# Kernel tuning notes

Hardware: AMD Instinct MI355X
Metric: run time of the kernel (lower is better)

## Reference

```python
import jax, jax.numpy as jnp
import numpy as np

B = 64
H = 768  # hidden_dim; x is [B, H, H], split along dim 1 into Q, D of [B, H//2, H]


def setup_inputs() -> dict:
    key = jax.random.key(0)
    kx, kw, kb = jax.random.split(key, 3)
    x = jax.random.normal(kx, (B, H, H), dtype=jnp.float32)
    # nn.Linear(H, H): weight [out, in], bias [out]
    W = jax.random.normal(kw, (H, H), dtype=jnp.float32) * (1.0 / np.sqrt(H))
    b = jax.random.normal(kb, (H,), dtype=jnp.float32) * 0.01
    return {"x": x, "W": W, "b": b}


def reference(x, W, b):
    T = H // 2
    Q = x[:, :T, :]          # [B, T, H]
    D = x[:, T:2 * T, :]     # [B, T, H]
    # Q = tanh(Linear(Q)); torch Linear: y = x @ W^T + b
    Q = jnp.tanh(jnp.einsum('bth,oh->bto', Q, W) + b)  # [B, T, H]
    D_t = jnp.swapaxes(D, 1, 2)                         # [B, H, T]
    L = jnp.einsum('bth,bsh->bts', Q, D)                # [B, T, T]
    A_Q = jnp.swapaxes(jax.nn.softmax(L, axis=1), 1, 2) # softmax over dim 1, then transpose -> [B, T, T]
    C_Q = jnp.matmul(D_t, A_Q)                          # [B, H, T]
    Q_t = jnp.swapaxes(Q, 1, 2)                         # [B, H, T]
    A_D = jax.nn.softmax(L, axis=2)                     # [B, T, T]
    C_D = jnp.matmul(jnp.concatenate((Q_t, C_Q), axis=1), A_D)  # [B, 2H, T]
    C_D_t = jnp.swapaxes(C_D, 1, 2)                     # [B, T, 2H]
    return jnp.concatenate((C_D_t, D), axis=2)          # [B, T, 3H]
```

## Files before the change

kernel.cpp:

```cpp
#include <hip/hip_runtime.h>


typedef __bf16 bf16x8 __attribute__((ext_vector_type(8)));
typedef __bf16 bf16x4 __attribute__((ext_vector_type(4)));
typedef float  f32x4  __attribute__((ext_vector_type(4)));

#define HH 768
#define TT 384

__device__ inline void split8(const float* __restrict__ p, bf16x8& hi, bf16x8& lo) {
    float4 f0 = *(const float4*)p;
    float4 f1 = *(const float4*)(p + 4);
    float f[8] = {f0.x, f0.y, f0.z, f0.w, f1.x, f1.y, f1.z, f1.w};
#pragma unroll
    for (int i = 0; i < 8; i++) {
        __bf16 h = (__bf16)f[i];
        hi[i] = h;
        lo[i] = (__bf16)(f[i] - (float)h);
    }
}

__device__ inline void gload16(const void* g, void* l) {
    __builtin_amdgcn_global_load_lds(
        (const __attribute__((address_space(1))) unsigned int*)g,
        (__attribute__((address_space(3))) unsigned int*)l, 16, 0, 0);
}

__global__ void prep_kernel(const float* __restrict__ x, __bf16* __restrict__ Dt,
                            float* __restrict__ out) {
    __shared__ float tile[32][33];
    int b = blockIdx.z;
    int h0 = blockIdx.x * 32, s0 = blockIdx.y * 32;
    int tx = threadIdx.x, ty = threadIdx.y;
    const float* src = x + ((size_t)b * HH + TT) * HH;
    float* outb = out + (size_t)b * TT * 2304;
#pragma unroll
    for (int j = 0; j < 4; j++) {
        int s = s0 + ty + 8 * j, h = h0 + tx;
        float v = src[(size_t)s * HH + h];
        tile[ty + 8 * j][tx] = v;
        outb[(size_t)s * 2304 + 1536 + h] = v;
    }
    __syncthreads();
    __bf16* Dtb = Dt + (size_t)b * HH * TT;
#pragma unroll
    for (int j = 0; j < 4; j++) {
        int h = h0 + ty + 8 * j, s = s0 + tx;
        Dtb[(size_t)h * TT + s] = (__bf16)tile[tx][ty + 8 * j];
    }
}

__global__ void splitW_kernel(const float* __restrict__ W, __bf16* __restrict__ Whi,
                              __bf16* __restrict__ Wlo) {
    int idx = blockIdx.x * 256 + threadIdx.x;
    bf16x8 h, l;
    split8(W + (size_t)idx * 8, h, l);
    *(bf16x8*)&Whi[(size_t)idx * 8] = h;
    *(bf16x8*)&Wlo[(size_t)idx * 8] = l;
}

__global__ __launch_bounds__(256) void gemm1_kernel(
    const float* __restrict__ x, const __bf16* __restrict__ Whi,
    const __bf16* __restrict__ Wlo, const float* __restrict__ bias,
    __bf16* __restrict__ Qhi, __bf16* __restrict__ Qlo, __bf16* __restrict__ M4) {
    __shared__ __bf16 Ah[128 * 32], Al[128 * 32], Bh[128 * 32], Bl[128 * 32];
    const int b = blockIdx.z;
    const int m_blk = blockIdx.y * 128, n_blk = blockIdx.x * 128;
    const int tid = threadIdx.x, lane = tid & 63, wave = tid >> 6;
    const int wm = wave >> 1, wn = wave & 1;
    const int r15 = lane & 15, quad = lane >> 4;
    const float* Abase = x + (size_t)b * HH * HH;
    f32x4 acc[4][4];
#pragma unroll
    for (int i = 0; i < 4; i++)
#pragma unroll
        for (int j = 0; j < 4; j++) acc[i][j] = (f32x4){0.f, 0.f, 0.f, 0.f};

    for (int k0 = 0; k0 < HH; k0 += 32) {
#pragma unroll
        for (int it = 0; it < 2; it++) {
            int c = it * 256 + tid;
            int r = c >> 2, q = c & 3;
            gload16(Whi + (size_t)(n_blk + r) * HH + k0 + q * 8, &Bh[c * 8]);
            gload16(Wlo + (size_t)(n_blk + r) * HH + k0 + q * 8, &Bl[c * 8]);
            bf16x8 h, l;
            split8(Abase + (size_t)(m_blk + r) * HH + k0 + q * 8, h, l);
            *(bf16x8*)&Ah[c * 8] = h;
            *(bf16x8*)&Al[c * 8] = l;
        }
        __syncthreads();
        bf16x8 ah[4], al[4], bh[4], bl[4];
#pragma unroll
        for (int i = 0; i < 4; i++) {
            int ra = (wm * 64 + i * 16 + r15) * 32 + quad * 8;
            ah[i] = *(const bf16x8*)&Ah[ra];
            al[i] = *(const bf16x8*)&Al[ra];
            int rb = (wn * 64 + i * 16 + r15) * 32 + quad * 8;
            bh[i] = *(const bf16x8*)&Bh[rb];
            bl[i] = *(const bf16x8*)&Bl[rb];
        }
#pragma unroll
        for (int i = 0; i < 4; i++)
#pragma unroll
            for (int j = 0; j < 4; j++) {
                acc[i][j] = __builtin_amdgcn_mfma_f32_16x16x32_bf16(ah[i], bh[j], acc[i][j], 0, 0, 0);
                acc[i][j] = __builtin_amdgcn_mfma_f32_16x16x32_bf16(ah[i], bl[j], acc[i][j], 0, 0, 0);
                acc[i][j] = __builtin_amdgcn_mfma_f32_16x16x32_bf16(al[i], bh[j], acc[i][j], 0, 0, 0);
            }
        __syncthreads();
    }
    __bf16* Qh = Qhi + (size_t)b * TT * HH;
    __bf16* Ql = Qlo + (size_t)b * TT * HH;
    __bf16* Mb = M4 + (size_t)b * 1536 * TT;
#pragma unroll
    for (int j = 0; j < 4; j++) {
        int col = n_blk + wn * 64 + j * 16 + r15;
        float bv = bias[col];
#pragma unroll
        for (int i = 0; i < 4; i++) {
            int row0 = m_blk + wm * 64 + i * 16 + quad * 4;
            bf16x4 mrow;
#pragma unroll
            for (int r = 0; r < 4; r++) {
                float v = tanhf(acc[i][j][r] + bv);
                __bf16 qh = (__bf16)v;
                Qh[(size_t)(row0 + r) * HH + col] = qh;
                Ql[(size_t)(row0 + r) * HH + col] = (__bf16)(v - (float)qh);
                mrow[r] = qh;
            }
            *(bf16x4*)&Mb[(size_t)col * TT + row0] = mrow;
        }
    }
}

__global__ __launch_bounds__(256) void gemm2_kernel(
    const __bf16* __restrict__ Qhi, const __bf16* __restrict__ Qlo,
    const float* __restrict__ x, float* __restrict__ L) {
    __shared__ __bf16 Ah[128 * 32], Al[128 * 32], Bh[128 * 32], Bl[128 * 32];
    const int b = blockIdx.z;
    const int m_blk = blockIdx.y * 128, n_blk = blockIdx.x * 128;
    const int tid = threadIdx.x, lane = tid & 63, wave = tid >> 6;
    const int wm = wave >> 1, wn = wave & 1;
    const int r15 = lane & 15, quad = lane >> 4;
    const __bf16* Qh = Qhi + (size_t)b * TT * HH;
    const __bf16* Ql = Qlo + (size_t)b * TT * HH;
    const float* Dbase = x + ((size_t)b * HH + TT) * HH;
    f32x4 acc[4][4];
#pragma unroll
    for (int i = 0; i < 4; i++)
#pragma unroll
        for (int j = 0; j < 4; j++) acc[i][j] = (f32x4){0.f, 0.f, 0.f, 0.f};

    for (int k0 = 0; k0 < HH; k0 += 32) {
#pragma unroll
        for (int it = 0; it < 2; it++) {
            int c = it * 256 + tid;
            int r = c >> 2, q = c & 3;
            gload16(Qh + (size_t)(m_blk + r) * HH + k0 + q * 8, &Ah[c * 8]);
            gload16(Ql + (size_t)(m_blk + r) * HH + k0 + q * 8, &Al[c * 8]);
            bf16x8 h, l;
            split8(Dbase + (size_t)(n_blk + r) * HH + k0 + q * 8, h, l);
            *(bf16x8*)&Bh[c * 8] = h;
            *(bf16x8*)&Bl[c * 8] = l;
        }
        __syncthreads();
        bf16x8 ah[4], al[4], bh[4], bl[4];
#pragma unroll
        for (int i = 0; i < 4; i++) {
            int ra = (wm * 64 + i * 16 + r15) * 32 + quad * 8;
            ah[i] = *(const bf16x8*)&Ah[ra];
            al[i] = *(const bf16x8*)&Al[ra];
            int rb = (wn * 64 + i * 16 + r15) * 32 + quad * 8;
            bh[i] = *(const bf16x8*)&Bh[rb];
            bl[i] = *(const bf16x8*)&Bl[rb];
        }
#pragma unroll
        for (int i = 0; i < 4; i++)
#pragma unroll
            for (int j = 0; j < 4; j++) {
                acc[i][j] = __builtin_amdgcn_mfma_f32_16x16x32_bf16(ah[i], bh[j], acc[i][j], 0, 0, 0);
                acc[i][j] = __builtin_amdgcn_mfma_f32_16x16x32_bf16(ah[i], bl[j], acc[i][j], 0, 0, 0);
                acc[i][j] = __builtin_amdgcn_mfma_f32_16x16x32_bf16(al[i], bh[j], acc[i][j], 0, 0, 0);
            }
        __syncthreads();
    }
    float* Lb = L + (size_t)b * TT * TT;
#pragma unroll
    for (int j = 0; j < 4; j++) {
        int col = n_blk + wn * 64 + j * 16 + r15;
#pragma unroll
        for (int i = 0; i < 4; i++) {
            int row0 = m_blk + wm * 64 + i * 16 + quad * 4;
#pragma unroll
            for (int r = 0; r < 4; r++) Lb[(size_t)(row0 + r) * TT + col] = acc[i][j][r];
        }
    }
}

__global__ void softmax_col_kernel(const float* __restrict__ L, __bf16* __restrict__ AQt) {
    int s = blockIdx.x, b = blockIdx.y;
    int tid = threadIdx.x;
    const float* Lb = L + (size_t)b * TT * TT;
    float v0 = Lb[(size_t)tid * TT + s];
    float v1 = Lb[(size_t)(tid + 128) * TT + s];
    float v2 = Lb[(size_t)(tid + 256) * TT + s];
    __shared__ float red[128];
    red[tid] = fmaxf(fmaxf(v0, v1), v2);
    __syncthreads();
    for (int off = 64; off > 0; off >>= 1) {
        if (tid < off) red[tid] = fmaxf(red[tid], red[tid + off]);
        __syncthreads();
    }
    float mx = red[0];
    __syncthreads();
    float e0 = __expf(v0 - mx), e1 = __expf(v1 - mx), e2 = __expf(v2 - mx);
    red[tid] = e0 + e1 + e2;
    __syncthreads();
    for (int off = 64; off > 0; off >>= 1) {
        if (tid < off) red[tid] += red[tid + off];
        __syncthreads();
    }
    float inv = 1.0f / red[0];
    __bf16* Ab = AQt + (size_t)b * TT * TT;
    Ab[(size_t)tid * TT + s] = (__bf16)(e0 * inv);
    Ab[(size_t)(tid + 128) * TT + s] = (__bf16)(e1 * inv);
    Ab[(size_t)(tid + 256) * TT + s] = (__bf16)(e2 * inv);
}

__global__ void softmax_row_kernel(const float* __restrict__ L, __bf16* __restrict__ ADt) {
    int t = blockIdx.x, b = blockIdx.y;
    int tid = threadIdx.x;
    const float* Lb = L + (size_t)b * TT * TT + (size_t)t * TT;
    float v0 = Lb[tid], v1 = Lb[tid + 128], v2 = Lb[tid + 256];
    __shared__ float red[128];
    red[tid] = fmaxf(fmaxf(v0, v1), v2);
    __syncthreads();
    for (int off = 64; off > 0; off >>= 1) {
        if (tid < off) red[tid] = fmaxf(red[tid], red[tid + off]);
        __syncthreads();
    }
    float mx = red[0];
    __syncthreads();
    float e0 = __expf(v0 - mx), e1 = __expf(v1 - mx), e2 = __expf(v2 - mx);
    red[tid] = e0 + e1 + e2;
    __syncthreads();
    for (int off = 64; off > 0; off >>= 1) {
        if (tid < off) red[tid] += red[tid + off];
        __syncthreads();
    }
    float inv = 1.0f / red[0];
    __bf16* Ab = ADt + (size_t)b * TT * TT;
    Ab[(size_t)tid * TT + t] = (__bf16)(e0 * inv);
    Ab[(size_t)(tid + 128) * TT + t] = (__bf16)(e1 * inv);
    Ab[(size_t)(tid + 256) * TT + t] = (__bf16)(e2 * inv);
}

__global__ __launch_bounds__(256) void gemm3_kernel(
    const __bf16* __restrict__ Dt, const __bf16* __restrict__ AQt,
    __bf16* __restrict__ M4) {
    __shared__ __bf16 As[128 * 32], Bs[128 * 32];
    const int b = blockIdx.z;
    const int m_blk = blockIdx.y * 128, n_blk = blockIdx.x * 128;
    const int tid = threadIdx.x, lane = tid & 63, wave = tid >> 6;
    const int wm = wave >> 1, wn = wave & 1;
    const int r15 = lane & 15, quad = lane >> 4;
    const __bf16* Ab = Dt + (size_t)b * HH * TT;
    const __bf16* Bb = AQt + (size_t)b * TT * TT;
    f32x4 acc[4][4];
#pragma unroll
    for (int i = 0; i < 4; i++)
#pragma unroll
        for (int j = 0; j < 4; j++) acc[i][j] = (f32x4){0.f, 0.f, 0.f, 0.f};

    for (int k0 = 0; k0 < TT; k0 += 32) {
#pragma unroll
        for (int it = 0; it < 2; it++) {
            int c = it * 256 + tid;
            int r = c >> 2, q = c & 3;
            gload16(Ab + (size_t)(m_blk + r) * TT + k0 + q * 8, &As[c * 8]);
            gload16(Bb + (size_t)(n_blk + r) * TT + k0 + q * 8, &Bs[c * 8]);
        }
        __syncthreads();
        bf16x8 a[4], bf[4];
#pragma unroll
        for (int i = 0; i < 4; i++) {
            a[i] = *(const bf16x8*)&As[(wm * 64 + i * 16 + r15) * 32 + quad * 8];
            bf[i] = *(const bf16x8*)&Bs[(wn * 64 + i * 16 + r15) * 32 + quad * 8];
        }
#pragma unroll
        for (int i = 0; i < 4; i++)
#pragma unroll
            for (int j = 0; j < 4; j++)
                acc[i][j] = __builtin_amdgcn_mfma_f32_16x16x32_bf16(a[i], bf[j], acc[i][j], 0, 0, 0);
        __syncthreads();
    }
    __bf16* Mb = M4 + (size_t)b * 1536 * TT;
#pragma unroll
    for (int j = 0; j < 4; j++) {
        int col = n_blk + wn * 64 + j * 16 + r15;
#pragma unroll
        for (int i = 0; i < 4; i++) {
            int row0 = m_blk + wm * 64 + i * 16 + quad * 4;
#pragma unroll
            for (int r = 0; r < 4; r++)
                Mb[(size_t)(768 + row0 + r) * TT + col] = (__bf16)acc[i][j][r];
        }
    }
}

__global__ __launch_bounds__(256) void gemm4_kernel(
    const __bf16* __restrict__ ADt, const __bf16* __restrict__ M4,
    float* __restrict__ out) {
    __shared__ __bf16 As[128 * 32], Bs[128 * 32];
    const int b = blockIdx.z;
    const int m_blk = blockIdx.y * 128, n_blk = blockIdx.x * 128;
    const int tid = threadIdx.x, lane = tid & 63, wave = tid >> 6;
    const int wm = wave >> 1, wn = wave & 1;
    const int r15 = lane & 15, quad = lane >> 4;
    const __bf16* Ab = ADt + (size_t)b * TT * TT;
    const __bf16* Bb = M4 + (size_t)b * 1536 * TT;
    f32x4 acc[4][4];
#pragma unroll
    for (int i = 0; i < 4; i++)
#pragma unroll
        for (int j = 0; j < 4; j++) acc[i][j] = (f32x4){0.f, 0.f, 0.f, 0.f};

    for (int k0 = 0; k0 < TT; k0 += 32) {
#pragma unroll
        for (int it = 0; it < 2; it++) {
            int c = it * 256 + tid;
            int r = c >> 2, q = c & 3;
            gload16(Ab + (size_t)(m_blk + r) * TT + k0 + q * 8, &As[c * 8]);
            gload16(Bb + (size_t)(n_blk + r) * TT + k0 + q * 8, &Bs[c * 8]);
        }
        __syncthreads();
        bf16x8 a[4], bf[4];
#pragma unroll
        for (int i = 0; i < 4; i++) {
            a[i] = *(const bf16x8*)&As[(wm * 64 + i * 16 + r15) * 32 + quad * 8];
            bf[i] = *(const bf16x8*)&Bs[(wn * 64 + i * 16 + r15) * 32 + quad * 8];
        }
#pragma unroll
        for (int i = 0; i < 4; i++)
#pragma unroll
            for (int j = 0; j < 4; j++)
                acc[i][j] = __builtin_amdgcn_mfma_f32_16x16x32_bf16(a[i], bf[j], acc[i][j], 0, 0, 0);
        __syncthreads();
    }
    float* outb = out + (size_t)b * TT * 2304;
#pragma unroll
    for (int j = 0; j < 4; j++) {
        int col = n_blk + wn * 64 + j * 16 + r15;
#pragma unroll
        for (int i = 0; i < 4; i++) {
            int row0 = m_blk + wm * 64 + i * 16 + quad * 4;
#pragma unroll
            for (int r = 0; r < 4; r++)
                outb[(size_t)(row0 + r) * 2304 + col] = acc[i][j][r];
        }
    }
}

extern "C" void kernel_launch(void* const* d_in, const int* in_sizes, int n_in,
                              void* d_out, int out_size, void* d_ws, size_t ws_size,
                              hipStream_t stream) {
    const float* x = (const float*)d_in[0];
    const float* W = (const float*)d_in[1];
    const float* bias = (const float*)d_in[2];
    float* out = (float*)d_out;
    char* ws = (char*)d_ws;

    __bf16* Qhi = (__bf16*)(ws + 0);
    __bf16* Qlo = (__bf16*)(ws + 37748736);
    __bf16* M4 = (__bf16*)(ws + 75497472);
    __bf16* Dt = (__bf16*)(ws + 150994944);
    float* L = (float*)(ws + 188743680);
    __bf16* AQt = (__bf16*)(ws + 0);
    __bf16* ADt = (__bf16*)(ws + 37748736);
    __bf16* Whi = (__bf16*)(ws + 188743680);
    __bf16* Wlo = Whi + 768 * 768;

    prep_kernel<<<dim3(24, 12, 64), dim3(32, 8), 0, stream>>>(x, Dt, out);
    splitW_kernel<<<288, 256, 0, stream>>>(W, Whi, Wlo);
    gemm1_kernel<<<dim3(6, 3, 64), 256, 0, stream>>>(x, Whi, Wlo, bias, Qhi, Qlo, M4);
    gemm2_kernel<<<dim3(3, 3, 64), 256, 0, stream>>>(Qhi, Qlo, x, L);
    softmax_col_kernel<<<dim3(384, 64), 128, 0, stream>>>(L, AQt);
    softmax_row_kernel<<<dim3(384, 64), 128, 0, stream>>>(L, ADt);
    gemm3_kernel<<<dim3(3, 6, 64), 256, 0, stream>>>(Dt, AQt, M4);
    gemm4_kernel<<<dim3(12, 3, 64), 256, 0, stream>>>(ADt, M4, out);
}
```

Baseline: 885.1 us.

## Coalesce softmax kernels and replace global_load_lds with register-staged loads

```diff
diff --git a/kernel.cpp b/kernel.cpp
--- a/kernel.cpp
+++ b/kernel.cpp
@@ -81,8 +81,10 @@
         for (int it = 0; it < 2; it++) {
             int c = it * 256 + tid;
             int r = c >> 2, q = c & 3;
-            gload16(Whi + (size_t)(n_blk + r) * HH + k0 + q * 8, &Bh[c * 8]);
-            gload16(Wlo + (size_t)(n_blk + r) * HH + k0 + q * 8, &Bl[c * 8]);
+            bf16x8 wh = *(const bf16x8*)&Whi[(size_t)(n_blk + r) * HH + k0 + q * 8];
+            bf16x8 wl = *(const bf16x8*)&Wlo[(size_t)(n_blk + r) * HH + k0 + q * 8];
+            *(bf16x8*)&Bh[c * 8] = wh;
+            *(bf16x8*)&Bl[c * 8] = wl;
             bf16x8 h, l;
             split8(Abase + (size_t)(m_blk + r) * HH + k0 + q * 8, h, l);
             *(bf16x8*)&Ah[c * 8] = h;
@@ -156,8 +158,10 @@
         for (int it = 0; it < 2; it++) {
             int c = it * 256 + tid;
             int r = c >> 2, q = c & 3;
-            gload16(Qh + (size_t)(m_blk + r) * HH + k0 + q * 8, &Ah[c * 8]);
-            gload16(Ql + (size_t)(m_blk + r) * HH + k0 + q * 8, &Al[c * 8]);
+            bf16x8 qh8 = *(const bf16x8*)&Qh[(size_t)(m_blk + r) * HH + k0 + q * 8];
+            bf16x8 ql8 = *(const bf16x8*)&Ql[(size_t)(m_blk + r) * HH + k0 + q * 8];
+            *(bf16x8*)&Ah[c * 8] = qh8;
+            *(bf16x8*)&Al[c * 8] = ql8;
             bf16x8 h, l;
             split8(Dbase + (size_t)(n_blk + r) * HH + k0 + q * 8, h, l);
             *(bf16x8*)&Bh[c * 8] = h;
@@ -198,61 +202,68 @@
 }
 
 __global__ void softmax_col_kernel(const float* __restrict__ L, __bf16* __restrict__ AQt) {
-    int s = blockIdx.x, b = blockIdx.y;
-    int tid = threadIdx.x;
+    int b = blockIdx.y;
+    int tx = threadIdx.x, ty = threadIdx.y;
+    int s = blockIdx.x * 64 + tx;
     const float* Lb = L + (size_t)b * TT * TT;
-    float v0 = Lb[(size_t)tid * TT + s];
-    float v1 = Lb[(size_t)(tid + 128) * TT + s];
-    float v2 = Lb[(size_t)(tid + 256) * TT + s];
-    __shared__ float red[128];
-    red[tid] = fmaxf(fmaxf(v0, v1), v2);
+    __shared__ float red[4][64];
+    float mx = -1e30f;
+    for (int t = ty; t < TT; t += 4) mx = fmaxf(mx, Lb[(size_t)t * TT + s]);
+    red[ty][tx] = mx;
     __syncthreads();
-    for (int off = 64; off > 0; off >>= 1) {
-        if (tid < off) red[tid] = fmaxf(red[tid], red[tid + off]);
-        __syncthreads();
-    }
-    float mx = red[0];
+    mx = fmaxf(fmaxf(red[0][tx], red[1][tx]), fmaxf(red[2][tx], red[3][tx]));
+    float sum = 0.f;
+    for (int t = ty; t < TT; t += 4) sum += __expf(Lb[(size_t)t * TT + s] - mx);
     __syncthreads();
-    float e0 = __expf(v0 - mx), e1 = __expf(v1 - mx), e2 = __expf(v2 - mx);
-    red[tid] = e0 + e1 + e2;
+    red[ty][tx] = sum;
     __syncthreads();
-    for (int off = 64; off > 0; off >>= 1) {
-        if (tid < off) red[tid] += red[tid + off];
-        __syncthreads();
-    }
-    float inv = 1.0f / red[0];
+    float inv = 1.0f / (red[0][tx] + red[1][tx] + red[2][tx] + red[3][tx]);
     __bf16* Ab = AQt + (size_t)b * TT * TT;
-    Ab[(size_t)tid * TT + s] = (__bf16)(e0 * inv);
-    Ab[(size_t)(tid + 128) * TT + s] = (__bf16)(e1 * inv);
-    Ab[(size_t)(tid + 256) * TT + s] = (__bf16)(e2 * inv);
+    for (int t = ty; t < TT; t += 4)
+        Ab[(size_t)t * TT + s] = (__bf16)(__expf(Lb[(size_t)t * TT + s] - mx) * inv);
 }
 
 __global__ void softmax_row_kernel(const float* __restrict__ L, __bf16* __restrict__ ADt) {
-    int t = blockIdx.x, b = blockIdx.y;
-    int tid = threadIdx.x;
-    const float* Lb = L + (size_t)b * TT * TT + (size_t)t * TT;
-    float v0 = Lb[tid], v1 = Lb[tid + 128], v2 = Lb[tid + 256];
-    __shared__ float red[128];
-    red[tid] = fmaxf(fmaxf(v0, v1), v2);
+    int b = blockIdx.y;
+    int t0 = blockIdx.x * 64;
+    int tx = threadIdx.x, ty = threadIdx.y;
+    int tid = ty * 64 + tx;
+    const float* Lb = L + (size_t)b * TT * TT;
+    __shared__ __bf16 ex[64][TT];
+    for (int rr = ty; rr < 64; rr += 4) {
+        const float* row = Lb + (size_t)(t0 + rr) * TT;
+        float v[6];
+        float mx = -1e30f;
+#pragma unroll
+        for (int k = 0; k < 6; k++) {
+            v[k] = row[tx + 64 * k];
+            mx = fmaxf(mx, v[k]);
+        }
+#pragma unroll
+        for (int off = 32; off > 0; off >>= 1) mx = fmaxf(mx, __shfl_xor(mx, off));
+        float sum = 0.f;
+#pragma unroll
+        for (int k = 0; k < 6; k++) {
+            v[k] = __expf(v[k] - mx);
+            sum += v[k];
+        }
+#pragma unroll
+        for (int off = 32; off > 0; off >>= 1) sum += __shfl_xor(sum, off);
+        float inv = 1.0f / sum;
+#pragma unroll
+        for (int k = 0; k < 6; k++) ex[rr][tx + 64 * k] = (__bf16)(v[k] * inv);
+    }
     __syncthreads();
-    for (int off = 64; off > 0; off >>= 1) {
-        if (tid < off) red[tid] = fmaxf(red[tid], red[tid + off]);
-        __syncthreads();
-    }
-    float mx = red[0];
-    __syncthreads();
-    float e0 = __expf(v0 - mx), e1 = __expf(v1 - mx), e2 = __expf(v2 - mx);
-    red[tid] = e0 + e1 + e2;
-    __syncthreads();
-    for (int off = 64; off > 0; off >>= 1) {
-        if (tid < off) red[tid] += red[tid + off];
-        __syncthreads();
-    }
-    float inv = 1.0f / red[0];
     __bf16* Ab = ADt + (size_t)b * TT * TT;
-    Ab[(size_t)tid * TT + t] = (__bf16)(e0 * inv);
-    Ab[(size_t)(tid + 128) * TT + t] = (__bf16)(e1 * inv);
-    Ab[(size_t)(tid + 256) * TT + t] = (__bf16)(e2 * inv);
+    for (int s = tid; s < TT; s += 256) {
+#pragma unroll
+        for (int j = 0; j < 8; j++) {
+            bf16x8 t8;
+#pragma unroll
+            for (int e = 0; e < 8; e++) t8[e] = ex[j * 8 + e][s];
+            *(bf16x8*)&Ab[(size_t)s * TT + t0 + j * 8] = t8;
+        }
+    }
 }
 
 __global__ __launch_bounds__(256) void gemm3_kernel(
@@ -384,8 +395,8 @@
     splitW_kernel<<<288, 256, 0, stream>>>(W, Whi, Wlo);
     gemm1_kernel<<<dim3(6, 3, 64), 256, 0, stream>>>(x, Whi, Wlo, bias, Qhi, Qlo, M4);
     gemm2_kernel<<<dim3(3, 3, 64), 256, 0, stream>>>(Qhi, Qlo, x, L);
-    softmax_col_kernel<<<dim3(384, 64), 128, 0, stream>>>(L, AQt);
-    softmax_row_kernel<<<dim3(384, 64), 128, 0, stream>>>(L, ADt);
+    softmax_col_kernel<<<dim3(6, 64), dim3(64, 4), 0, stream>>>(L, AQt);
+    softmax_row_kernel<<<dim3(6, 64), dim3(64, 4), 0, stream>>>(L, ADt);
     gemm3_kernel<<<dim3(3, 6, 64), 256, 0, stream>>>(Dt, AQt, M4);
     gemm4_kernel<<<dim3(12, 3, 64), 256, 0, stream>>>(ADt, M4, out);
 }
```

Measured after the change: 815.8 us. 1.08x faster.
